# Performance work log

Measured on AMD Instinct MI355X. Metric: run time of the kernel, lower is better.

## Reference

```python
import jax, jax.numpy as jnp
import numpy as np

# attn_reps = "8x0n+30x1n": per head channel C = 8 scalars + 30 Lorentz four-vectors (4 each) = 128
N_SCALARS, N_VECTORS = 8, 30
ETA = jnp.diag(jnp.array([1.0, -1.0, -1.0, -1.0], dtype=jnp.float32))  # Minkowski metric


def _quat_to_rot(q):
    # q: (M,4) unit quaternions -> (M,3,3) rotation matrices
    w, x, y, z = q[:, 0], q[:, 1], q[:, 2], q[:, 3]
    r0 = jnp.stack([1 - 2 * (y * y + z * z), 2 * (x * y - w * z), 2 * (x * z + w * y)], axis=-1)
    r1 = jnp.stack([2 * (x * y + w * z), 1 - 2 * (x * x + z * z), 2 * (y * z - w * x)], axis=-1)
    r2 = jnp.stack([2 * (x * z - w * y), 2 * (y * z + w * x), 1 - 2 * (x * x + y * y)], axis=-1)
    return jnp.stack([r0, r1, r2], axis=-2)


def _random_lorentz(key, M):
    # random proper Lorentz transforms: boost(beta) @ blockdiag(1, R)
    k1, k2 = jax.random.split(key)
    quat = jax.random.normal(k1, (M, 4), dtype=jnp.float32)
    quat = quat / jnp.linalg.norm(quat, axis=-1, keepdims=True)
    R = _quat_to_rot(quat)  # (M,3,3)
    beta = jax.random.uniform(k2, (M, 3), minval=-1.0, maxval=1.0, dtype=jnp.float32) * (0.6 / np.sqrt(3.0))
    b2 = jnp.sum(beta * beta, axis=-1)  # (M,), < 0.36
    gamma = 1.0 / jnp.sqrt(1.0 - b2)
    n = beta / jnp.sqrt(jnp.maximum(b2, 1e-12))[:, None]
    gb = gamma[:, None] * beta  # (M,3)
    top = jnp.concatenate([gamma[:, None], gb], axis=-1)[:, None, :]  # (M,1,4)
    spatial = jnp.eye(3, dtype=jnp.float32) + (gamma - 1.0)[:, None, None] * n[:, :, None] * n[:, None, :]
    bottom = jnp.concatenate([gb[:, :, None], spatial], axis=-1)  # (M,3,4)
    B = jnp.concatenate([top, bottom], axis=-2)  # (M,4,4) boost
    rot4 = jnp.zeros((M, 4, 4), dtype=jnp.float32).at[:, 0, 0].set(1.0).at[:, 1:, 1:].set(R)
    return jnp.einsum('mij,mjk->mik', B, rot4)


def setup_inputs() -> dict:
    key = jax.random.key(0)
    kq, kk, kv, kl = jax.random.split(key, 4)
    B, H, N, C = 8, 8, 1024, 128
    q = jax.random.normal(kq, (B, H, N, C), dtype=jnp.float32)
    k = jax.random.normal(kk, (B, H, N, C), dtype=jnp.float32)
    v = jax.random.normal(kv, (B, H, N, C), dtype=jnp.float32)
    L = _random_lorentz(kl, B * N).reshape(B, N, 4, 4)
    return {"q_local": q, "k_local": k, "v_local": v, "lframes_matrices": L}


def _transform(x, M):
    # TensorRepsTransform: scalars pass through, four-vectors get v' = M v (per particle)
    # x: (B,H,N,C), M: (B,N,4,4)
    s = x[..., :N_SCALARS]
    vec = x[..., N_SCALARS:].reshape(x.shape[:-1] + (N_VECTORS, 4))
    vec = jnp.einsum('bnij,bhnvj->bhnvi', M, vec)
    return jnp.concatenate([s, vec.reshape(x.shape[:-1] + (N_VECTORS * 4,))], axis=-1)


def reference(q_local, k_local, v_local, lframes_matrices):
    C = q_local.shape[-1]
    # InverseLFrames: Lorentz inverse  Lambda^{-1} = eta Lambda^T eta
    inv = jnp.einsum('ij,bnkj,kl->bnil', ETA, lframes_matrices, ETA)
    # LowerIndices: lower the output index -> eta @ Lambda^{-1}
    lower_inv = jnp.einsum('ij,bnjk->bnik', ETA, inv)
    q_g = _transform(q_local, inv)
    k_g = _transform(k_local, lower_inv)
    v_g = _transform(v_local, inv)
    # standard SDPA (scale 1/sqrt(C))
    scores = jnp.einsum('bhqc,bhkc->bhqk', q_g, k_g) * (1.0 / np.sqrt(C))
    attn = jax.nn.softmax(scores, axis=-1)
    out_g = jnp.einsum('bhqk,bhkc->bhqc', attn, v_g)
    # back to local frame with Lambda itself
    return _transform(out_g, lframes_matrices)
```

## Files before the change

### kernel.cpp

```cpp
#include <hip/hip_runtime.h>
#include <math.h>

typedef _Float16 f16;
typedef _Float16 f16x4 __attribute__((ext_vector_type(4)));
typedef _Float16 f16x8 __attribute__((ext_vector_type(8)));
typedef float    f32x4 __attribute__((ext_vector_type(4)));

#define NSEQ 1024
#define CD   128
#define LT   136


__global__ __launch_bounds__(256)
void ipa_pre(const float* __restrict__ kg, const float* __restrict__ vg,
             const float* __restrict__ Lm, f16* __restrict__ khs, f16* __restrict__ vhs)
{
    __shared__ float LL[64 * 16];
    __shared__ __align__(16) f16 Kt[64 * LT];
    __shared__ __align__(16) f16 Vt[64 * LT];
    const int bx = blockIdx.x, nt = blockIdx.y, tid = threadIdx.x;
    const int bh = ((bx & 7) << 3) | (bx >> 3);
    const int b  = bh >> 3;
    const float* Lb = Lm + ((size_t)b * NSEQ + nt * 64) * 16;
    for (int t = tid; t < 64 * 16; t += 256) LL[t] = Lb[t];
    __syncthreads();

    const size_t base = ((size_t)bh * NSEQ + nt * 64) * CD;
    #pragma unroll
    for (int it = 0; it < 8; ++it) {
        int g = it * 256 + tid;
        int row = g >> 5, cg = g & 31;
        size_t idx = base + row * CD + cg * 4;
        const float* Lr = &LL[row * 16];
        float4 xk = *(const float4*)(kg + idx);
        float4 xv = *(const float4*)(vg + idx);
        float4 yk = xk, yv = xv;
        if (cg >= 2) {
            float t0 = xk.x, t1 = -xk.y, t2 = -xk.z, t3 = -xk.w;
            yk.x = Lr[0]*t0 + Lr[4]*t1 + Lr[8] *t2 + Lr[12]*t3;
            yk.y = Lr[1]*t0 + Lr[5]*t1 + Lr[9] *t2 + Lr[13]*t3;
            yk.z = Lr[2]*t0 + Lr[6]*t1 + Lr[10]*t2 + Lr[14]*t3;
            yk.w = Lr[3]*t0 + Lr[7]*t1 + Lr[11]*t2 + Lr[15]*t3;
            t0 = xv.x; t1 = -xv.y; t2 = -xv.z; t3 = -xv.w;
            yv.x =  (Lr[0]*t0 + Lr[4]*t1 + Lr[8] *t2 + Lr[12]*t3);
            yv.y = -(Lr[1]*t0 + Lr[5]*t1 + Lr[9] *t2 + Lr[13]*t3);
            yv.z = -(Lr[2]*t0 + Lr[6]*t1 + Lr[10]*t2 + Lr[14]*t3);
            yv.w = -(Lr[3]*t0 + Lr[7]*t1 + Lr[11]*t2 + Lr[15]*t3);
        }
        f16x4 hk = {(f16)yk.x, (f16)yk.y, (f16)yk.z, (f16)yk.w};
        f16x4 hv = {(f16)yv.x, (f16)yv.y, (f16)yv.z, (f16)yv.w};
        *(f16x4*)&Kt[row * LT + cg * 4] = hk;
        *(f16x4*)&Vt[row * LT + cg * 4] = hv;
    }
    __syncthreads();

    f16* kout = khs + (size_t)bh * 131072 + (size_t)nt * 4 * 4 * 512;
    #pragma unroll
    for (int it = 0; it < 4; ++it) {
        int slot = it * 256 + tid;
        int g16l = slot >> 8, cs = (slot >> 6) & 3, L = slot & 63;
        int lq = L & 15, quad = L >> 4;
        int keyl = ((g16l >> 1) << 5) + ((lq >> 2) << 3) + ((g16l & 1) << 2) + (lq & 3);
        f16x8 kv = *(const f16x8*)&Kt[keyl * LT + cs * 32 + quad * 8];
        *(f16x8*)(kout + (g16l * 4 + cs) * 512 + L * 8) = kv;
    }
    f16* vout = vhs + (size_t)bh * 131072 + (size_t)nt * 2 * 8 * 512;
    #pragma unroll
    for (int it = 0; it < 4; ++it) {
        int slot = it * 256 + tid;
        int k32l = slot >> 9, cb = (slot >> 6) & 7, L = slot & 63;
        int lq = L & 15, quad = L >> 4;
        int c = cb * 16 + lq;
        f16x8 o;
        #pragma unroll
        for (int j = 0; j < 8; ++j)
            o[j] = Vt[(k32l * 32 + quad * 8 + j) * LT + c];
        *(f16x8*)(vout + (k32l * 8 + cb) * 512 + L * 8) = o;
    }
}

__global__ __launch_bounds__(128, 2)
void ipa_attn(const float* __restrict__ qg, const f16* __restrict__ khs,
              const f16* __restrict__ vhs, const float* __restrict__ Lm,
              float* __restrict__ out)
{
    const int n = blockIdx.x;
    const int bh = ((n & 7) << 3) | ((n >> 3) & 7);
    const int b  = bh >> 3;
    const int tid = threadIdx.x;
    const int w = tid >> 6, lane = tid & 63, lq = lane & 15, quad = lane >> 4;
    const int qw = (n >> 6) * 2 + w;
    const int q0 = qw * 32;
    const f16* kbh = khs + (size_t)bh * 131072;
    const f16* vbh = vhs + (size_t)bh * 131072;
    const float sc2 = 0.12751744154226873f;

    f16x8 qf[2][4];
    #pragma unroll
    for (int u = 0; u < 2; ++u) {
        int qrow = q0 + u * 16 + lq;
        const float* Lr = Lm + ((size_t)b * NSEQ + qrow) * 16;
        const float* qp = qg + ((size_t)bh * NSEQ + qrow) * CD;
        float Lv[16];
        #pragma unroll
        for (int i = 0; i < 4; ++i) *(float4*)&Lv[i*4] = *(const float4*)(Lr + i*4);
        #pragma unroll
        for (int cs = 0; cs < 4; ++cs) {
            int c0 = cs * 32 + quad * 8;
            float4 x0 = *(const float4*)(qp + c0);
            float4 x1 = *(const float4*)(qp + c0 + 4);
            if (c0 >= 8) {
                float t0 = x0.x, t1 = -x0.y, t2 = -x0.z, t3 = -x0.w;
                float4 y;
                y.x =  (Lv[0]*t0 + Lv[4]*t1 + Lv[8] *t2 + Lv[12]*t3);
                y.y = -(Lv[1]*t0 + Lv[5]*t1 + Lv[9] *t2 + Lv[13]*t3);
                y.z = -(Lv[2]*t0 + Lv[6]*t1 + Lv[10]*t2 + Lv[14]*t3);
                y.w = -(Lv[3]*t0 + Lv[7]*t1 + Lv[11]*t2 + Lv[15]*t3);
                x0 = y;
                t0 = x1.x; t1 = -x1.y; t2 = -x1.z; t3 = -x1.w;
                y.x =  (Lv[0]*t0 + Lv[4]*t1 + Lv[8] *t2 + Lv[12]*t3);
                y.y = -(Lv[1]*t0 + Lv[5]*t1 + Lv[9] *t2 + Lv[13]*t3);
                y.z = -(Lv[2]*t0 + Lv[6]*t1 + Lv[10]*t2 + Lv[14]*t3);
                y.w = -(Lv[3]*t0 + Lv[7]*t1 + Lv[11]*t2 + Lv[15]*t3);
                x1 = y;
            }
            qf[u][cs] = (f16x8){(f16)(x0.x*sc2), (f16)(x0.y*sc2), (f16)(x0.z*sc2), (f16)(x0.w*sc2),
                                (f16)(x1.x*sc2), (f16)(x1.y*sc2), (f16)(x1.z*sc2), (f16)(x1.w*sc2)};
        }
    }

    f32x4 oacc[2][8];
    #pragma unroll
    for (int u = 0; u < 2; ++u)
        #pragma unroll
        for (int cb = 0; cb < 8; ++cb) oacc[u][cb] = (f32x4){0.f, 0.f, 0.f, 0.f};
    float mrun[2] = {-1e30f, -1e30f}, lrun[2] = {0.f, 0.f};

    for (int it = 0; it < 16; ++it) {
        const f16* kp = kbh + (size_t)it * 16 * 512;
        f16x8 kf[4][4];
        #pragma unroll
        for (int g = 0; g < 4; ++g)
            #pragma unroll
            for (int cs = 0; cs < 4; ++cs)
                kf[g][cs] = *(const f16x8*)(kp + (g * 4 + cs) * 512 + lane * 8);

        f32x4 s[2][4];
        #pragma unroll
        for (int u = 0; u < 2; ++u)
            #pragma unroll
            for (int g = 0; g < 4; ++g) s[u][g] = (f32x4){0.f, 0.f, 0.f, 0.f};
        #pragma unroll
        for (int g = 0; g < 4; ++g)
            #pragma unroll
            for (int cs = 0; cs < 4; ++cs) {
                s[0][g] = __builtin_amdgcn_mfma_f32_16x16x32_f16(kf[g][cs], qf[0][cs], s[0][g], 0, 0, 0);
                s[1][g] = __builtin_amdgcn_mfma_f32_16x16x32_f16(kf[g][cs], qf[1][cs], s[1][g], 0, 0, 0);
            }

        const f16* vp = vbh + (size_t)it * 2 * 8 * 512;
        f16x8 vf[2][8];
        #pragma unroll
        for (int k2 = 0; k2 < 2; ++k2)
            #pragma unroll
            for (int cb = 0; cb < 8; ++cb)
                vf[k2][cb] = *(const f16x8*)(vp + (k2 * 8 + cb) * 512 + lane * 8);

        f16x8 pf[2][2];
        float alpha[2];
        #pragma unroll
        for (int u = 0; u < 2; ++u) {
            float mx = -1e30f;
            #pragma unroll
            for (int g = 0; g < 4; ++g)
                mx = fmaxf(mx, fmaxf(fmaxf(s[u][g].x, s[u][g].y), fmaxf(s[u][g].z, s[u][g].w)));
            mx = fmaxf(mx, __shfl_xor(mx, 16, 64));
            mx = fmaxf(mx, __shfl_xor(mx, 32, 64));
            float mnew = fmaxf(mrun[u], mx);
            alpha[u] = exp2f(mrun[u] - mnew);
            float p[16], rs = 0.f;
            #pragma unroll
            for (int g = 0; g < 4; ++g) {
                p[g*4+0] = exp2f(s[u][g].x - mnew);
                p[g*4+1] = exp2f(s[u][g].y - mnew);
                p[g*4+2] = exp2f(s[u][g].z - mnew);
                p[g*4+3] = exp2f(s[u][g].w - mnew);
                rs += (p[g*4+0] + p[g*4+1]) + (p[g*4+2] + p[g*4+3]);
            }
            rs += __shfl_xor(rs, 16, 64);
            rs += __shfl_xor(rs, 32, 64);
            lrun[u] = alpha[u] * lrun[u] + rs;
            mrun[u] = mnew;
            pf[u][0] = (f16x8){(f16)p[0],(f16)p[1],(f16)p[2],(f16)p[3],(f16)p[4],(f16)p[5],(f16)p[6],(f16)p[7]};
            pf[u][1] = (f16x8){(f16)p[8],(f16)p[9],(f16)p[10],(f16)p[11],(f16)p[12],(f16)p[13],(f16)p[14],(f16)p[15]};
        }
        #pragma unroll
        for (int u = 0; u < 2; ++u)
            #pragma unroll
            for (int cb = 0; cb < 8; ++cb) oacc[u][cb] *= alpha[u];
        #pragma unroll
        for (int k2 = 0; k2 < 2; ++k2)
            #pragma unroll
            for (int cb = 0; cb < 8; ++cb) {
                oacc[0][cb] = __builtin_amdgcn_mfma_f32_16x16x32_f16(vf[k2][cb], pf[0][k2], oacc[0][cb], 0, 0, 0);
                oacc[1][cb] = __builtin_amdgcn_mfma_f32_16x16x32_f16(vf[k2][cb], pf[1][k2], oacc[1][cb], 0, 0, 0);
            }
    }

    #pragma unroll
    for (int u = 0; u < 2; ++u) {
        int qrow = q0 + u * 16 + lq;
        float invl = 1.0f / lrun[u];
        const float* Lr = Lm + ((size_t)b * NSEQ + qrow) * 16;
        float* ob = out + ((size_t)bh * NSEQ + qrow) * CD;
        #pragma unroll
        for (int cb = 0; cb < 8; ++cb) {
            int c0 = cb * 16 + quad * 4;
            float o0 = oacc[u][cb].x*invl, o1 = oacc[u][cb].y*invl;
            float o2 = oacc[u][cb].z*invl, o3 = oacc[u][cb].w*invl;
            float4 r;
            if (c0 >= 8) {
                r.x = Lr[0] *o0 + Lr[1] *o1 + Lr[2] *o2 + Lr[3] *o3;
                r.y = Lr[4] *o0 + Lr[5] *o1 + Lr[6] *o2 + Lr[7] *o3;
                r.z = Lr[8] *o0 + Lr[9] *o1 + Lr[10]*o2 + Lr[11]*o3;
                r.w = Lr[12]*o0 + Lr[13]*o1 + Lr[14]*o2 + Lr[15]*o3;
            } else {
                r.x = o0; r.y = o1; r.z = o2; r.w = o3;
            }
            *(float4*)(ob + c0) = r;
        }
    }
}

extern "C" void kernel_launch(void* const* d_in, const int* in_sizes, int n_in,
                              void* d_out, int out_size, void* d_ws, size_t ws_size,
                              hipStream_t stream) {
    const float* q = (const float*)d_in[0];
    const float* k = (const float*)d_in[1];
    const float* v = (const float*)d_in[2];
    const float* L = (const float*)d_in[3];
    float* o = (float*)d_out;
    f16* khs = (f16*)d_ws;
    f16* vhs = khs + (size_t)64 * 131072;
    dim3 grid1(64, 16);
    ipa_pre<<<grid1, 256, 0, stream>>>(k, v, L, khs, vhs);
    ipa_attn<<<1024, 128, 0, stream>>>(q, khs, vhs, L, o);
}
```

Before: 194.0 us.

## Split key range across two waves per query tile and merge via LDS

Each attention block now runs four waves instead of two. Two waves share a query tile and each processes half of the key sequence, and their softmax partial states (output accumulators, running max, running sum) are merged through shared memory at the end. This doubles the number of waves per CU to hide memory latency and shortens each wave's serial loop. The online-softmax rescale is also skipped whenever no lane's max increased. The cost is extra LDS traffic, a block barrier, and the merge arithmetic, and half of the waves sit idle during the epilogue.

```diff
diff --git a/kernel.cpp b/kernel.cpp
--- a/kernel.cpp
+++ b/kernel.cpp
@@ -79,17 +79,19 @@
     }
 }
 
-__global__ __launch_bounds__(128, 2)
+__global__ __launch_bounds__(256, 4)
 void ipa_attn(const float* __restrict__ qg, const f16* __restrict__ khs,
               const f16* __restrict__ vhs, const float* __restrict__ Lm,
               float* __restrict__ out)
 {
+    __shared__ __align__(16) float mrg[2][64][68];
     const int n = blockIdx.x;
     const int bh = ((n & 7) << 3) | ((n >> 3) & 7);
     const int b  = bh >> 3;
     const int tid = threadIdx.x;
     const int w = tid >> 6, lane = tid & 63, lq = lane & 15, quad = lane >> 4;
-    const int qw = (n >> 6) * 2 + w;
+    const int qw = (n >> 6) * 2 + (w >> 1);
+    const int kh = w & 1;
     const int q0 = qw * 32;
     const f16* kbh = khs + (size_t)bh * 131072;
     const f16* vbh = vhs + (size_t)bh * 131072;
@@ -136,7 +138,7 @@
         for (int cb = 0; cb < 8; ++cb) oacc[u][cb] = (f32x4){0.f, 0.f, 0.f, 0.f};
     float mrun[2] = {-1e30f, -1e30f}, lrun[2] = {0.f, 0.f};
 
-    for (int it = 0; it < 16; ++it) {
+    for (int it = kh * 8; it < kh * 8 + 8; ++it) {
         const f16* kp = kbh + (size_t)it * 16 * 512;
         f16x8 kf[4][4];
         #pragma unroll
@@ -167,7 +169,6 @@
                 vf[k2][cb] = *(const f16x8*)(vp + (k2 * 8 + cb) * 512 + lane * 8);
 
         f16x8 pf[2][2];
-        float alpha[2];
         #pragma unroll
         for (int u = 0; u < 2; ++u) {
             float mx = -1e30f;
@@ -177,7 +178,13 @@
             mx = fmaxf(mx, __shfl_xor(mx, 16, 64));
             mx = fmaxf(mx, __shfl_xor(mx, 32, 64));
             float mnew = fmaxf(mrun[u], mx);
-            alpha[u] = exp2f(mrun[u] - mnew);
+            if (!__all(mx <= mrun[u])) {
+                float alpha = exp2f(mrun[u] - mnew);
+                lrun[u] *= alpha;
+                #pragma unroll
+                for (int cb = 0; cb < 8; ++cb) oacc[u][cb] *= alpha;
+                mrun[u] = mnew;
+            }
             float p[16], rs = 0.f;
             #pragma unroll
             for (int g = 0; g < 4; ++g) {
@@ -189,15 +196,10 @@
             }
             rs += __shfl_xor(rs, 16, 64);
             rs += __shfl_xor(rs, 32, 64);
-            lrun[u] = alpha[u] * lrun[u] + rs;
-            mrun[u] = mnew;
+            lrun[u] += rs;
             pf[u][0] = (f16x8){(f16)p[0],(f16)p[1],(f16)p[2],(f16)p[3],(f16)p[4],(f16)p[5],(f16)p[6],(f16)p[7]};
             pf[u][1] = (f16x8){(f16)p[8],(f16)p[9],(f16)p[10],(f16)p[11],(f16)p[12],(f16)p[13],(f16)p[14],(f16)p[15]};
         }
-        #pragma unroll
-        for (int u = 0; u < 2; ++u)
-            #pragma unroll
-            for (int cb = 0; cb < 8; ++cb) oacc[u][cb] *= alpha[u];
         #pragma unroll
         for (int k2 = 0; k2 < 2; ++k2)
             #pragma unroll
@@ -207,17 +209,37 @@
             }
     }
 
+    if (kh) {
+        float* dst = &mrg[w >> 1][lane][0];
+        #pragma unroll
+        for (int u = 0; u < 2; ++u)
+            #pragma unroll
+            for (int cb = 0; cb < 8; ++cb)
+                *(f32x4*)&dst[u * 32 + cb * 4] = oacc[u][cb];
+        dst[64] = mrun[0]; dst[65] = lrun[0]; dst[66] = mrun[1]; dst[67] = lrun[1];
+    }
+    __syncthreads();
+    if (kh) return;
+
+    const float* src = &mrg[w >> 1][lane][0];
     #pragma unroll
     for (int u = 0; u < 2; ++u) {
+        float mB = src[64 + u * 2], lB = src[65 + u * 2];
+        float m  = fmaxf(mrun[u], mB);
+        float eA = exp2f(mrun[u] - m), eB = exp2f(mB - m);
+        float l  = lrun[u] * eA + lB * eB;
+        float invl = 1.0f / l;
         int qrow = q0 + u * 16 + lq;
-        float invl = 1.0f / lrun[u];
         const float* Lr = Lm + ((size_t)b * NSEQ + qrow) * 16;
         float* ob = out + ((size_t)bh * NSEQ + qrow) * CD;
         #pragma unroll
         for (int cb = 0; cb < 8; ++cb) {
+            f32x4 oB = *(const f32x4*)&src[u * 32 + cb * 4];
             int c0 = cb * 16 + quad * 4;
-            float o0 = oacc[u][cb].x*invl, o1 = oacc[u][cb].y*invl;
-            float o2 = oacc[u][cb].z*invl, o3 = oacc[u][cb].w*invl;
+            float o0 = (oacc[u][cb].x * eA + oB.x * eB) * invl;
+            float o1 = (oacc[u][cb].y * eA + oB.y * eB) * invl;
+            float o2 = (oacc[u][cb].z * eA + oB.z * eB) * invl;
+            float o3 = (oacc[u][cb].w * eA + oB.w * eB) * invl;
             float4 r;
             if (c0 >= 8) {
                 r.x = Lr[0] *o0 + Lr[1] *o1 + Lr[2] *o2 + Lr[3] *o3;
@@ -244,5 +266,5 @@
     f16* vhs = khs + (size_t)64 * 131072;
     dim3 grid1(64, 16);
     ipa_pre<<<grid1, 256, 0, stream>>>(k, v, L, khs, vhs);
-    ipa_attn<<<1024, 128, 0, stream>>>(q, khs, vhs, L, o);
+    ipa_attn<<<1024, 256, 0, stream>>>(q, khs, vhs, L, o);
 }
```

New measurement: 505.0 us. +160.3%, slower.

## Stage K/V tiles in LDS via async double-buffered loads shared by four waves

Applied to the files above, without the earlier changes.

The attention kernel now runs four waves per block, each handling 32 queries, over a 128-query slab. The block cooperatively copies each 64-key K and V tile from global memory into double-buffered LDS with global_load_lds, so four waves share one fetch instead of two. The next tile is prefetched while the current one is computed. The online-softmax rescale of the output accumulators is also skipped when the row max does not increase, checked per wave. In exchange the kernel uses 64 KB of LDS per block and adds a barrier each iteration, which may limit occupancy.

```diff
diff --git a/kernel.cpp b/kernel.cpp
--- a/kernel.cpp
+++ b/kernel.cpp
@@ -5,6 +5,9 @@
 typedef _Float16 f16x4 __attribute__((ext_vector_type(4)));
 typedef _Float16 f16x8 __attribute__((ext_vector_type(8)));
 typedef float    f32x4 __attribute__((ext_vector_type(4)));
+
+typedef const __attribute__((address_space(1))) void gv_t;
+typedef __attribute__((address_space(3))) void lv_t;
 
 #define NSEQ 1024
 #define CD   128
@@ -79,21 +82,38 @@
     }
 }
 
-__global__ __launch_bounds__(128, 2)
+__global__ __launch_bounds__(256, 2)
 void ipa_attn(const float* __restrict__ qg, const f16* __restrict__ khs,
               const f16* __restrict__ vhs, const float* __restrict__ Lm,
               float* __restrict__ out)
 {
+    __shared__ __align__(16) f16 sK[2][8192];
+    __shared__ __align__(16) f16 sV[2][8192];
     const int n = blockIdx.x;
     const int bh = ((n & 7) << 3) | ((n >> 3) & 7);
     const int b  = bh >> 3;
     const int tid = threadIdx.x;
     const int w = tid >> 6, lane = tid & 63, lq = lane & 15, quad = lane >> 4;
-    const int qw = (n >> 6) * 2 + w;
-    const int q0 = qw * 32;
+    const int qblk = n >> 6;
+    const int q0 = qblk * 128 + w * 32;
     const f16* kbh = khs + (size_t)bh * 131072;
     const f16* vbh = vhs + (size_t)bh * 131072;
     const float sc2 = 0.12751744154226873f;
+
+    auto stage = [&](int nb, int it) {
+        const char* kp = (const char*)(kbh + (size_t)it * 8192);
+        const char* vp = (const char*)(vbh + (size_t)it * 8192);
+        char* kd = (char*)&sK[nb][0];
+        char* vd = (char*)&sV[nb][0];
+        #pragma unroll
+        for (int j = 0; j < 4; ++j) {
+            int off = (w * 4 + j) * 1024;
+            __builtin_amdgcn_global_load_lds((gv_t*)(kp + off + lane * 16),
+                                             (lv_t*)(kd + off), 16, 0, 0);
+            __builtin_amdgcn_global_load_lds((gv_t*)(vp + off + lane * 16),
+                                             (lv_t*)(vd + off), 16, 0, 0);
+        }
+    };
 
     f16x8 qf[2][4];
     #pragma unroll
@@ -136,14 +156,21 @@
         for (int cb = 0; cb < 8; ++cb) oacc[u][cb] = (f32x4){0.f, 0.f, 0.f, 0.f};
     float mrun[2] = {-1e30f, -1e30f}, lrun[2] = {0.f, 0.f};
 
+    stage(0, 0);
+
     for (int it = 0; it < 16; ++it) {
-        const f16* kp = kbh + (size_t)it * 16 * 512;
+        const int cur = it & 1;
+        __syncthreads();
+        if (it < 15) stage(cur ^ 1, it + 1);
+
+        const f16* kb = &sK[cur][0];
+        const f16* vb = &sV[cur][0];
         f16x8 kf[4][4];
         #pragma unroll
         for (int g = 0; g < 4; ++g)
             #pragma unroll
             for (int cs = 0; cs < 4; ++cs)
-                kf[g][cs] = *(const f16x8*)(kp + (g * 4 + cs) * 512 + lane * 8);
+                kf[g][cs] = *(const f16x8*)&kb[(g * 4 + cs) * 512 + lane * 8];
 
         f32x4 s[2][4];
         #pragma unroll
@@ -158,16 +185,14 @@
                 s[1][g] = __builtin_amdgcn_mfma_f32_16x16x32_f16(kf[g][cs], qf[1][cs], s[1][g], 0, 0, 0);
             }
 
-        const f16* vp = vbh + (size_t)it * 2 * 8 * 512;
         f16x8 vf[2][8];
         #pragma unroll
         for (int k2 = 0; k2 < 2; ++k2)
             #pragma unroll
             for (int cb = 0; cb < 8; ++cb)
-                vf[k2][cb] = *(const f16x8*)(vp + (k2 * 8 + cb) * 512 + lane * 8);
+                vf[k2][cb] = *(const f16x8*)&vb[(k2 * 8 + cb) * 512 + lane * 8];
 
         f16x8 pf[2][2];
-        float alpha[2];
         #pragma unroll
         for (int u = 0; u < 2; ++u) {
             float mx = -1e30f;
@@ -177,7 +202,13 @@
             mx = fmaxf(mx, __shfl_xor(mx, 16, 64));
             mx = fmaxf(mx, __shfl_xor(mx, 32, 64));
             float mnew = fmaxf(mrun[u], mx);
-            alpha[u] = exp2f(mrun[u] - mnew);
+            if (!__all(mx <= mrun[u])) {
+                float alpha = exp2f(mrun[u] - mnew);
+                lrun[u] *= alpha;
+                #pragma unroll
+                for (int cb = 0; cb < 8; ++cb) oacc[u][cb] *= alpha;
+                mrun[u] = mnew;
+            }
             float p[16], rs = 0.f;
             #pragma unroll
             for (int g = 0; g < 4; ++g) {
@@ -189,15 +220,10 @@
             }
             rs += __shfl_xor(rs, 16, 64);
             rs += __shfl_xor(rs, 32, 64);
-            lrun[u] = alpha[u] * lrun[u] + rs;
-            mrun[u] = mnew;
+            lrun[u] += rs;
             pf[u][0] = (f16x8){(f16)p[0],(f16)p[1],(f16)p[2],(f16)p[3],(f16)p[4],(f16)p[5],(f16)p[6],(f16)p[7]};
             pf[u][1] = (f16x8){(f16)p[8],(f16)p[9],(f16)p[10],(f16)p[11],(f16)p[12],(f16)p[13],(f16)p[14],(f16)p[15]};
         }
-        #pragma unroll
-        for (int u = 0; u < 2; ++u)
-            #pragma unroll
-            for (int cb = 0; cb < 8; ++cb) oacc[u][cb] *= alpha[u];
         #pragma unroll
         for (int k2 = 0; k2 < 2; ++k2)
             #pragma unroll
@@ -244,5 +270,5 @@
     f16* vhs = khs + (size_t)64 * 131072;
     dim3 grid1(64, 16);
     ipa_pre<<<grid1, 256, 0, stream>>>(k, v, L, khs, vhs);
-    ipa_attn<<<1024, 128, 0, stream>>>(q, khs, vhs, L, o);
+    ipa_attn<<<512, 256, 0, stream>>>(q, khs, vhs, L, o);
 }
```

Result: no change. 190.3 us, median of 2 (-1.9%).

## Fuse K/V Lorentz transform into attention kernel with LDS staging and prefetch

Applied to the files above, without the earlier changes.

Removes the separate preprocessing kernel and its fp16 workspace. Each 256-thread block now handles 128 queries and loads fp32 K/V tiles itself, applies the frame transform, and stages them in shared memory, with register prefetch of the next tile overlapping compute. It also skips the online-softmax rescale when no row's max grows and defers the row-sum cross-lane reduction to the end. In exchange, every query block repeats the K/V transform and fp32 loads (8x per head instead of once), and each tile needs extra barriers and scalar transposed LDS writes for V.

```diff
diff --git a/kernel.cpp b/kernel.cpp
--- a/kernel.cpp
+++ b/kernel.cpp
@@ -8,92 +8,32 @@
 
 #define NSEQ 1024
 #define CD   128
-#define LT   136
-
-
-__global__ __launch_bounds__(256)
-void ipa_pre(const float* __restrict__ kg, const float* __restrict__ vg,
-             const float* __restrict__ Lm, f16* __restrict__ khs, f16* __restrict__ vhs)
+#define KSTR 136
+#define VSTR 72
+
+__global__ __launch_bounds__(256, 2)
+void ipa_fused(const float* __restrict__ qg, const float* __restrict__ kg,
+               const float* __restrict__ vg, const float* __restrict__ Lm,
+               float* __restrict__ out)
 {
-    __shared__ float LL[64 * 16];
-    __shared__ __align__(16) f16 Kt[64 * LT];
-    __shared__ __align__(16) f16 Vt[64 * LT];
-    const int bx = blockIdx.x, nt = blockIdx.y, tid = threadIdx.x;
-    const int bh = ((bx & 7) << 3) | (bx >> 3);
-    const int b  = bh >> 3;
-    const float* Lb = Lm + ((size_t)b * NSEQ + nt * 64) * 16;
-    for (int t = tid; t < 64 * 16; t += 256) LL[t] = Lb[t];
-    __syncthreads();
-
-    const size_t base = ((size_t)bh * NSEQ + nt * 64) * CD;
-    #pragma unroll
-    for (int it = 0; it < 8; ++it) {
-        int g = it * 256 + tid;
-        int row = g >> 5, cg = g & 31;
-        size_t idx = base + row * CD + cg * 4;
-        const float* Lr = &LL[row * 16];
-        float4 xk = *(const float4*)(kg + idx);
-        float4 xv = *(const float4*)(vg + idx);
-        float4 yk = xk, yv = xv;
-        if (cg >= 2) {
-            float t0 = xk.x, t1 = -xk.y, t2 = -xk.z, t3 = -xk.w;
-            yk.x = Lr[0]*t0 + Lr[4]*t1 + Lr[8] *t2 + Lr[12]*t3;
-            yk.y = Lr[1]*t0 + Lr[5]*t1 + Lr[9] *t2 + Lr[13]*t3;
-            yk.z = Lr[2]*t0 + Lr[6]*t1 + Lr[10]*t2 + Lr[14]*t3;
-            yk.w = Lr[3]*t0 + Lr[7]*t1 + Lr[11]*t2 + Lr[15]*t3;
-            t0 = xv.x; t1 = -xv.y; t2 = -xv.z; t3 = -xv.w;
-            yv.x =  (Lr[0]*t0 + Lr[4]*t1 + Lr[8] *t2 + Lr[12]*t3);
-            yv.y = -(Lr[1]*t0 + Lr[5]*t1 + Lr[9] *t2 + Lr[13]*t3);
-            yv.z = -(Lr[2]*t0 + Lr[6]*t1 + Lr[10]*t2 + Lr[14]*t3);
-            yv.w = -(Lr[3]*t0 + Lr[7]*t1 + Lr[11]*t2 + Lr[15]*t3);
-        }
-        f16x4 hk = {(f16)yk.x, (f16)yk.y, (f16)yk.z, (f16)yk.w};
-        f16x4 hv = {(f16)yv.x, (f16)yv.y, (f16)yv.z, (f16)yv.w};
-        *(f16x4*)&Kt[row * LT + cg * 4] = hk;
-        *(f16x4*)&Vt[row * LT + cg * 4] = hv;
-    }
-    __syncthreads();
-
-    f16* kout = khs + (size_t)bh * 131072 + (size_t)nt * 4 * 4 * 512;
-    #pragma unroll
-    for (int it = 0; it < 4; ++it) {
-        int slot = it * 256 + tid;
-        int g16l = slot >> 8, cs = (slot >> 6) & 3, L = slot & 63;
-        int lq = L & 15, quad = L >> 4;
-        int keyl = ((g16l >> 1) << 5) + ((lq >> 2) << 3) + ((g16l & 1) << 2) + (lq & 3);
-        f16x8 kv = *(const f16x8*)&Kt[keyl * LT + cs * 32 + quad * 8];
-        *(f16x8*)(kout + (g16l * 4 + cs) * 512 + L * 8) = kv;
-    }
-    f16* vout = vhs + (size_t)bh * 131072 + (size_t)nt * 2 * 8 * 512;
-    #pragma unroll
-    for (int it = 0; it < 4; ++it) {
-        int slot = it * 256 + tid;
-        int k32l = slot >> 9, cb = (slot >> 6) & 7, L = slot & 63;
-        int lq = L & 15, quad = L >> 4;
-        int c = cb * 16 + lq;
-        f16x8 o;
-        #pragma unroll
-        for (int j = 0; j < 8; ++j)
-            o[j] = Vt[(k32l * 32 + quad * 8 + j) * LT + c];
-        *(f16x8*)(vout + (k32l * 8 + cb) * 512 + L * 8) = o;
-    }
-}
-
-__global__ __launch_bounds__(128, 2)
-void ipa_attn(const float* __restrict__ qg, const f16* __restrict__ khs,
-              const f16* __restrict__ vhs, const float* __restrict__ Lm,
-              float* __restrict__ out)
-{
+    __shared__ __align__(16) f16 Kt[64 * KSTR];
+    __shared__ __align__(16) f16 Vt[128 * VSTR];
     const int n = blockIdx.x;
     const int bh = ((n & 7) << 3) | ((n >> 3) & 7);
     const int b  = bh >> 3;
     const int tid = threadIdx.x;
     const int w = tid >> 6, lane = tid & 63, lq = lane & 15, quad = lane >> 4;
-    const int qw = (n >> 6) * 2 + w;
-    const int q0 = qw * 32;
-    const f16* kbh = khs + (size_t)bh * 131072;
-    const f16* vbh = vhs + (size_t)bh * 131072;
+    const int qblk = n >> 6;
+    const int q0 = qblk * 128 + w * 32;
     const float sc2 = 0.12751744154226873f;
+    const int kperm = ((lq >> 2) << 3) | (lq & 3);
+
+    const int krow = tid >> 2;
+    const int cq   = tid & 3;
+    const float* kgb = kg + ((size_t)bh * NSEQ) * CD + cq * 32;
+    const float* vgb = vg + ((size_t)bh * NSEQ) * CD + cq * 32;
+
+    float4 kx[8], vx[8];
 
     f16x8 qf[2][4];
     #pragma unroll
@@ -129,6 +69,68 @@
         }
     }
 
+    auto load_k = [&](int t) {
+        const float* kp = kgb + ((size_t)t * 64 + krow) * CD;
+        #pragma unroll
+        for (int j = 0; j < 8; ++j) kx[j] = *(const float4*)(kp + j * 4);
+    };
+    auto load_v = [&](int t) {
+        const float* vp = vgb + ((size_t)t * 64 + krow) * CD;
+        #pragma unroll
+        for (int j = 0; j < 8; ++j) vx[j] = *(const float4*)(vp + j * 4);
+    };
+    auto xform_write = [&](int t) {
+        int key = t * 64 + krow;
+        const float* Lr = Lm + ((size_t)b * NSEQ + key) * 16;
+        float Lv[16];
+        #pragma unroll
+        for (int i = 0; i < 4; ++i) *(float4*)&Lv[i*4] = *(const float4*)(Lr + i*4);
+        #pragma unroll
+        for (int jp = 0; jp < 4; ++jp) {
+            float4 a0 = kx[jp*2], a1 = kx[jp*2+1];
+            float4 b0 = vx[jp*2], b1 = vx[jp*2+1];
+            if (!(cq == 0 && jp == 0)) {
+                float t0 = a0.x, t1 = -a0.y, t2 = -a0.z, t3 = -a0.w;
+                float4 y;
+                y.x = Lv[0]*t0 + Lv[4]*t1 + Lv[8] *t2 + Lv[12]*t3;
+                y.y = Lv[1]*t0 + Lv[5]*t1 + Lv[9] *t2 + Lv[13]*t3;
+                y.z = Lv[2]*t0 + Lv[6]*t1 + Lv[10]*t2 + Lv[14]*t3;
+                y.w = Lv[3]*t0 + Lv[7]*t1 + Lv[11]*t2 + Lv[15]*t3;
+                a0 = y;
+                t0 = a1.x; t1 = -a1.y; t2 = -a1.z; t3 = -a1.w;
+                y.x = Lv[0]*t0 + Lv[4]*t1 + Lv[8] *t2 + Lv[12]*t3;
+                y.y = Lv[1]*t0 + Lv[5]*t1 + Lv[9] *t2 + Lv[13]*t3;
+                y.z = Lv[2]*t0 + Lv[6]*t1 + Lv[10]*t2 + Lv[14]*t3;
+                y.w = Lv[3]*t0 + Lv[7]*t1 + Lv[11]*t2 + Lv[15]*t3;
+                a1 = y;
+                t0 = b0.x; t1 = -b0.y; t2 = -b0.z; t3 = -b0.w;
+                y.x =  (Lv[0]*t0 + Lv[4]*t1 + Lv[8] *t2 + Lv[12]*t3);
+                y.y = -(Lv[1]*t0 + Lv[5]*t1 + Lv[9] *t2 + Lv[13]*t3);
+                y.z = -(Lv[2]*t0 + Lv[6]*t1 + Lv[10]*t2 + Lv[14]*t3);
+                y.w = -(Lv[3]*t0 + Lv[7]*t1 + Lv[11]*t2 + Lv[15]*t3);
+                b0 = y;
+                t0 = b1.x; t1 = -b1.y; t2 = -b1.z; t3 = -b1.w;
+                y.x =  (Lv[0]*t0 + Lv[4]*t1 + Lv[8] *t2 + Lv[12]*t3);
+                y.y = -(Lv[1]*t0 + Lv[5]*t1 + Lv[9] *t2 + Lv[13]*t3);
+                y.z = -(Lv[2]*t0 + Lv[6]*t1 + Lv[10]*t2 + Lv[14]*t3);
+                y.w = -(Lv[3]*t0 + Lv[7]*t1 + Lv[11]*t2 + Lv[15]*t3);
+                b1 = y;
+            }
+            int c0 = cq * 32 + jp * 8;
+            f16x8 hk = {(f16)a0.x,(f16)a0.y,(f16)a0.z,(f16)a0.w,
+                        (f16)a1.x,(f16)a1.y,(f16)a1.z,(f16)a1.w};
+            *(f16x8*)&Kt[krow * KSTR + c0] = hk;
+            Vt[(c0+0)*VSTR + krow] = (f16)b0.x;
+            Vt[(c0+1)*VSTR + krow] = (f16)b0.y;
+            Vt[(c0+2)*VSTR + krow] = (f16)b0.z;
+            Vt[(c0+3)*VSTR + krow] = (f16)b0.w;
+            Vt[(c0+4)*VSTR + krow] = (f16)b1.x;
+            Vt[(c0+5)*VSTR + krow] = (f16)b1.y;
+            Vt[(c0+6)*VSTR + krow] = (f16)b1.z;
+            Vt[(c0+7)*VSTR + krow] = (f16)b1.w;
+        }
+    };
+
     f32x4 oacc[2][8];
     #pragma unroll
     for (int u = 0; u < 2; ++u)
@@ -136,14 +138,19 @@
         for (int cb = 0; cb < 8; ++cb) oacc[u][cb] = (f32x4){0.f, 0.f, 0.f, 0.f};
     float mrun[2] = {-1e30f, -1e30f}, lrun[2] = {0.f, 0.f};
 
-    for (int it = 0; it < 16; ++it) {
-        const f16* kp = kbh + (size_t)it * 16 * 512;
+    load_k(0); load_v(0);
+    xform_write(0);
+    __syncthreads();
+
+    for (int t = 0; t < 16; ++t) {
         f16x8 kf[4][4];
         #pragma unroll
-        for (int g = 0; g < 4; ++g)
+        for (int g = 0; g < 4; ++g) {
+            int keyl = ((g >> 1) << 5) + ((g & 1) << 2) + kperm;
             #pragma unroll
             for (int cs = 0; cs < 4; ++cs)
-                kf[g][cs] = *(const f16x8*)(kp + (g * 4 + cs) * 512 + lane * 8);
+                kf[g][cs] = *(const f16x8*)&Kt[keyl * KSTR + cs * 32 + quad * 8];
+        }
 
         f32x4 s[2][4];
         #pragma unroll
@@ -157,17 +164,9 @@
                 s[0][g] = __builtin_amdgcn_mfma_f32_16x16x32_f16(kf[g][cs], qf[0][cs], s[0][g], 0, 0, 0);
                 s[1][g] = __builtin_amdgcn_mfma_f32_16x16x32_f16(kf[g][cs], qf[1][cs], s[1][g], 0, 0, 0);
             }
-
-        const f16* vp = vbh + (size_t)it * 2 * 8 * 512;
-        f16x8 vf[2][8];
-        #pragma unroll
-        for (int k2 = 0; k2 < 2; ++k2)
-            #pragma unroll
-            for (int cb = 0; cb < 8; ++cb)
-                vf[k2][cb] = *(const f16x8*)(vp + (k2 * 8 + cb) * 512 + lane * 8);
+        if (t < 15) load_k(t + 1);
 
         f16x8 pf[2][2];
-        float alpha[2];
         #pragma unroll
         for (int u = 0; u < 2; ++u) {
             float mx = -1e30f;
@@ -177,7 +176,13 @@
             mx = fmaxf(mx, __shfl_xor(mx, 16, 64));
             mx = fmaxf(mx, __shfl_xor(mx, 32, 64));
             float mnew = fmaxf(mrun[u], mx);
-            alpha[u] = exp2f(mrun[u] - mnew);
+            if (!__all(mx <= mrun[u])) {
+                float alpha = exp2f(mrun[u] - mnew);
+                lrun[u] *= alpha;
+                #pragma unroll
+                for (int cb = 0; cb < 8; ++cb) oacc[u][cb] *= alpha;
+                mrun[u] = mnew;
+            }
             float p[16], rs = 0.f;
             #pragma unroll
             for (int g = 0; g < 4; ++g) {
@@ -187,17 +192,18 @@
                 p[g*4+3] = exp2f(s[u][g].w - mnew);
                 rs += (p[g*4+0] + p[g*4+1]) + (p[g*4+2] + p[g*4+3]);
             }
-            rs += __shfl_xor(rs, 16, 64);
-            rs += __shfl_xor(rs, 32, 64);
-            lrun[u] = alpha[u] * lrun[u] + rs;
-            mrun[u] = mnew;
+            lrun[u] += rs;
             pf[u][0] = (f16x8){(f16)p[0],(f16)p[1],(f16)p[2],(f16)p[3],(f16)p[4],(f16)p[5],(f16)p[6],(f16)p[7]};
             pf[u][1] = (f16x8){(f16)p[8],(f16)p[9],(f16)p[10],(f16)p[11],(f16)p[12],(f16)p[13],(f16)p[14],(f16)p[15]};
         }
-        #pragma unroll
-        for (int u = 0; u < 2; ++u)
-            #pragma unroll
-            for (int cb = 0; cb < 8; ++cb) oacc[u][cb] *= alpha[u];
+        if (t < 15) load_v(t + 1);
+
+        f16x8 vf[2][8];
+        #pragma unroll
+        for (int k2 = 0; k2 < 2; ++k2)
+            #pragma unroll
+            for (int cb = 0; cb < 8; ++cb)
+                vf[k2][cb] = *(const f16x8*)&Vt[(cb * 16 + lq) * VSTR + k2 * 32 + quad * 8];
         #pragma unroll
         for (int k2 = 0; k2 < 2; ++k2)
             #pragma unroll
@@ -205,12 +211,21 @@
                 oacc[0][cb] = __builtin_amdgcn_mfma_f32_16x16x32_f16(vf[k2][cb], pf[0][k2], oacc[0][cb], 0, 0, 0);
                 oacc[1][cb] = __builtin_amdgcn_mfma_f32_16x16x32_f16(vf[k2][cb], pf[1][k2], oacc[1][cb], 0, 0, 0);
             }
+
+        if (t < 15) {
+            __syncthreads();
+            xform_write(t + 1);
+            __syncthreads();
+        }
     }
 
     #pragma unroll
     for (int u = 0; u < 2; ++u) {
+        float l = lrun[u];
+        l += __shfl_xor(l, 16, 64);
+        l += __shfl_xor(l, 32, 64);
+        float invl = 1.0f / l;
         int qrow = q0 + u * 16 + lq;
-        float invl = 1.0f / lrun[u];
         const float* Lr = Lm + ((size_t)b * NSEQ + qrow) * 16;
         float* ob = out + ((size_t)bh * NSEQ + qrow) * CD;
         #pragma unroll
@@ -240,9 +255,5 @@
     const float* v = (const float*)d_in[2];
     const float* L = (const float*)d_in[3];
     float* o = (float*)d_out;
-    f16* khs = (f16*)d_ws;
-    f16* vhs = khs + (size_t)64 * 131072;
-    dim3 grid1(64, 16);
-    ipa_pre<<<grid1, 256, 0, stream>>>(k, v, L, khs, vhs);
-    ipa_attn<<<1024, 128, 0, stream>>>(q, khs, vhs, L, o);
+    ipa_fused<<<512, 256, 0, stream>>>(q, k, v, L, o);
 }
```

Measured after the change: 218.4 us. +12.6%, slower.
